# Kernel optimization log

Measured on AMD Instinct MI355X. Metric: run time of the kernel, lower is better.

Reference implementation:

```python
import jax, jax.numpy as jnp
import numpy as np

NUM_ITEMS = 5
DIM = 1024
BATCH = 2048
NUM_PAIR = NUM_ITEMS * (NUM_ITEMS - 1)  # 20
NUM_RESULTS = 120  # 5!

# Off-diagonal ordered pairs in row-major flatten order (i*N + j, i != j).
_mask = ~np.eye(NUM_ITEMS, dtype=bool)
_IDX_I, _IDX_J = np.nonzero(_mask)  # each length NUM_PAIR
IDX_I = jnp.asarray(_IDX_I)
IDX_J = jnp.asarray(_IDX_J)


def setup_inputs() -> dict:
    key = jax.random.key(0)
    k1, k2, k3, k4, k5 = jax.random.split(key, 5)
    s_pw = 1.0 / np.sqrt(2 * DIM)
    s_cls = 1.0 / np.sqrt(NUM_PAIR * DIM)
    return {
        "embeds": jax.random.normal(k1, (BATCH, NUM_ITEMS, DIM), dtype=jnp.float32),
        "pw_w": jax.random.uniform(k2, (DIM, 2 * DIM), dtype=jnp.float32, minval=-s_pw, maxval=s_pw),
        "pw_b": jax.random.uniform(k3, (DIM,), dtype=jnp.float32, minval=-s_pw, maxval=s_pw),
        "cls_w": jax.random.uniform(k4, (NUM_RESULTS, NUM_PAIR * DIM), dtype=jnp.float32, minval=-s_cls, maxval=s_cls),
        "cls_b": jax.random.uniform(k5, (NUM_RESULTS,), dtype=jnp.float32, minval=-s_cls, maxval=s_cls),
    }


def reference(embeds, pw_w, pw_b, cls_w, cls_b):
    # Gather the two halves of each ordered off-diagonal pair directly
    # (equivalent to expand/cat/mask-select in the torch code).
    e_i = embeds[:, IDX_I, :]  # [B, P, D] : rep_1 (row item)
    e_j = embeds[:, IDX_J, :]  # [B, P, D] : rep_2 (col item)
    # pairwise_layer on concat(e_i, e_j): split weight to avoid the cat.
    w1 = pw_w[:, :DIM]
    w2 = pw_w[:, DIM:]
    pair = jnp.einsum('bpd,kd->bpk', e_i, w1) + jnp.einsum('bpd,kd->bpk', e_j, w2) + pw_b  # [B, P, D]
    flat = pair.reshape(pair.shape[0], -1)  # [B, P*D]
    return flat @ cls_w.T + cls_b  # [B, NUM_RESULTS]
```

## Files before the change

### kernel.cpp

```cpp
#include <hip/hip_runtime.h>


#define NR 120
#define KXX 5120
#define PM_SLICE (2048*128)
#define PF_SLICE (128*5120)

typedef __attribute__((ext_vector_type(8))) short bf8;
typedef __attribute__((ext_vector_type(4))) float f4;

__device__ __forceinline__ unsigned int f2bf(float f) {
    unsigned int x = __builtin_bit_cast(unsigned int, f);
    return (x + 0x7fffu + ((x >> 16) & 1u)) >> 16;
}
__device__ __forceinline__ float bf2f(unsigned short u) {
    unsigned int x = ((unsigned int)u) << 16;
    return __builtin_bit_cast(float, x);
}

__global__ __launch_bounds__(256) void k_prep(const float* __restrict__ cls_w,
                                              unsigned short* __restrict__ C2R) {
    const int col = blockIdx.x, half = blockIdx.y, t = threadIdx.x;
    const int n = col >> 7, r = col & 127;
    unsigned short* dst = C2R + (size_t)col * 2048 + half * 1024 + t * 4;
    if (r >= NR) { *(unsigned long long*)dst = 0ull; return; }
    const float* base = cls_w + (size_t)r * 20480 + t * 4;
    float sx = 0, sy = 0, sz = 0, sw = 0;
    if (half == 0) {
        #pragma unroll
        for (int q = 0; q < 4; q++) {
            float4 v = *(const float4*)(base + (4 * n + q) * 1024);
            sx += v.x; sy += v.y; sz += v.z; sw += v.w;
        }
    } else {
        #pragma unroll
        for (int i = 0; i < 5; i++) {
            if (i == n) continue;
            int q = (n > i) ? (n - 1) : n;
            float4 v = *(const float4*)(base + (4 * i + q) * 1024);
            sx += v.x; sy += v.y; sz += v.z; sw += v.w;
        }
    }
    unsigned long long pk = (unsigned long long)f2bf(sx)
                          | ((unsigned long long)f2bf(sy) << 16)
                          | ((unsigned long long)f2bf(sz) << 32)
                          | ((unsigned long long)f2bf(sw) << 48);
    *(unsigned long long*)dst = pk;
}

__global__ __launch_bounds__(256) void k_wprep(const float* __restrict__ pw_w,
                                               unsigned short* __restrict__ Afold) {
    __shared__ float T[64][65];
    const int d0 = blockIdx.x * 64, kt0 = blockIdx.y * 64;
    const int h = blockIdx.y >> 4, kr0 = (blockIdx.y & 15) * 64;
    const int t = threadIdx.x;
    #pragma unroll
    for (int lp = 0; lp < 4; lp++) {
        int lk = lp * 16 + (t >> 4);
        float4 v = *(const float4*)(pw_w + (size_t)(kr0 + lk) * 2048 + h * 1024 + d0 + (t & 15) * 4);
        T[lk][(t & 15) * 4 + 0] = v.x; T[lk][(t & 15) * 4 + 1] = v.y;
        T[lk][(t & 15) * 4 + 2] = v.z; T[lk][(t & 15) * 4 + 3] = v.w;
    }
    __syncthreads();
    #pragma unroll
    for (int wp = 0; wp < 2; wp++) {
        int ld = wp * 32 + (t >> 3);
        int lk2 = (t & 7) * 8;
        uint4 o;
        o.x = f2bf(T[lk2 + 0][ld]) | (f2bf(T[lk2 + 1][ld]) << 16);
        o.y = f2bf(T[lk2 + 2][ld]) | (f2bf(T[lk2 + 3][ld]) << 16);
        o.z = f2bf(T[lk2 + 4][ld]) | (f2bf(T[lk2 + 5][ld]) << 16);
        o.w = f2bf(T[lk2 + 6][ld]) | (f2bf(T[lk2 + 7][ld]) << 16);
        *(uint4*)(Afold + (size_t)(d0 + ld) * 2048 + kt0 + lk2) = o;
    }
}

__global__ __launch_bounds__(256) void k_const(const unsigned short* __restrict__ C2R,
                                               const float* __restrict__ pw_b,
                                               const float* __restrict__ cls_b,
                                               float* __restrict__ constv) {
    const int r = blockIdx.x, t = threadIdx.x;
    float acc = 0.f;
    for (int k = t; k < 1024; k += 256) {
        float s = 0.f;
        #pragma unroll
        for (int n = 0; n < 5; n++) s += bf2f(C2R[(size_t)(n * 128 + r) * 2048 + k]);
        acc += s * pw_b[k];
    }
    __shared__ float red[256];
    red[t] = acc; __syncthreads();
    for (int s2 = 128; s2 > 0; s2 >>= 1) {
        if (t < s2) red[t] += red[t + s2];
        __syncthreads();
    }
    if (t == 0) constv[r] = cls_b[r] + red[0];
}

__global__ __launch_bounds__(256) void k_fold(const unsigned short* __restrict__ Afold,
                                              const unsigned short* __restrict__ C2R,
                                              float* __restrict__ Pf, int kchunk) {
    __shared__ __align__(16) unsigned char smem[65536];
    unsigned short* Al = (unsigned short*)smem;
    unsigned short* Bl = Al + 128 * 64;
    const int d0 = blockIdx.x * 128, n = blockIdx.y;
    const int kc0 = blockIdx.z * kchunk;
    const int t = threadIdx.x, lane = t & 63, wv = t >> 6;
    const int wm = wv >> 1, wn = wv & 1;
    const int rr = t >> 3, f = t & 7;

    f4 acc[4][4];
    #pragma unroll
    for (int i = 0; i < 4; i++)
        #pragma unroll
        for (int j = 0; j < 4; j++) acc[i][j] = (f4){0.f, 0.f, 0.f, 0.f};

    const unsigned short* Ag = Afold + (size_t)d0 * 2048 + kc0;
    const unsigned short* Bg = C2R + (size_t)(n * 128) * 2048 + kc0;
    uint4 ra[4], rb[4];
    #pragma unroll
    for (int p = 0; p < 4; p++) {
        ra[p] = *(const uint4*)(Ag + (size_t)(p * 32 + rr) * 2048 + f * 8);
        rb[p] = *(const uint4*)(Bg + (size_t)(p * 32 + rr) * 2048 + f * 8);
    }
    const int nst = kchunk >> 6;
    for (int kt = 0; kt < nst; kt++) {
        if (kt) __syncthreads();
        #pragma unroll
        for (int p = 0; p < 4; p++) {
            int row = p * 32 + rr;
            int slot = f ^ (row & 7);
            *(uint4*)(Al + row * 64 + slot * 8) = ra[p];
            *(uint4*)(Bl + row * 64 + slot * 8) = rb[p];
        }
        __syncthreads();
        if (kt + 1 < nst) {
            int kb = (kt + 1) * 64;
            #pragma unroll
            for (int p = 0; p < 4; p++) {
                ra[p] = *(const uint4*)(Ag + (size_t)(p * 32 + rr) * 2048 + kb + f * 8);
                rb[p] = *(const uint4*)(Bg + (size_t)(p * 32 + rr) * 2048 + kb + f * 8);
            }
        }
        #pragma unroll
        for (int s = 0; s < 2; s++) {
            bf8 af[4], bq[4];
            #pragma unroll
            for (int ff = 0; ff < 4; ff++) {
                int rowa = wm * 64 + ff * 16 + (lane & 15);
                int sla = (s * 4 + (lane >> 4)) ^ (rowa & 7);
                af[ff] = *reinterpret_cast<const bf8*>(Al + rowa * 64 + sla * 8);
                int rowb = wn * 64 + ff * 16 + (lane & 15);
                int slb = (s * 4 + (lane >> 4)) ^ (rowb & 7);
                bq[ff] = *reinterpret_cast<const bf8*>(Bl + rowb * 64 + slb * 8);
            }
            #pragma unroll
            for (int i = 0; i < 4; i++)
                #pragma unroll
                for (int j = 0; j < 4; j++)
                    acc[i][j] = __builtin_amdgcn_mfma_f32_16x16x32_bf16(af[i], bq[j], acc[i][j], 0, 0, 0);
        }
    }
    __syncthreads();
    float* T = (float*)smem;
    #pragma unroll
    for (int i = 0; i < 4; i++) {
        int slog = wm * 16 + i * 4 + (lane >> 4);
        #pragma unroll
        for (int j = 0; j < 4; j++) {
            int c = wn * 64 + j * 16 + (lane & 15);
            int sphy = slog ^ ((c & 7) << 2);
            *(f4*)(T + (size_t)c * 128 + sphy * 4) = acc[i][j];
        }
    }
    __syncthreads();
    float* dst = Pf + (size_t)blockIdx.z * PF_SLICE + n * 1024 + d0;
    #pragma unroll
    for (int pass = 0; pass < 4; pass++) {
        int c = pass * 32 + (t >> 3);
        #pragma unroll
        for (int u = 0; u < 4; u++) {
            int slog = (t & 7) + u * 8;
            int sphy = slog ^ ((c & 7) << 2);
            float4 v = *(const float4*)(T + (size_t)c * 128 + sphy * 4);
            *(float4*)(dst + (size_t)c * KXX + slog * 4) = v;
        }
    }
}

__global__ __launch_bounds__(256) void k_foldred(const float* __restrict__ Pf,
                                                 unsigned short* __restrict__ WTt,
                                                 int ksf) {
    int i4 = blockIdx.x * 256 + threadIdx.x;
    const float4* p = (const float4*)Pf;
    float4 s = p[i4];
    for (int ks = 1; ks < ksf; ks++) {
        float4 v = p[(size_t)ks * (PF_SLICE / 4) + i4];
        s.x += v.x; s.y += v.y; s.z += v.z; s.w += v.w;
    }
    unsigned long long pk = (unsigned long long)f2bf(s.x)
                          | ((unsigned long long)f2bf(s.y) << 16)
                          | ((unsigned long long)f2bf(s.z) << 32)
                          | ((unsigned long long)f2bf(s.w) << 48);
    *(unsigned long long*)(WTt + (size_t)i4 * 4) = pk;
}

__global__ __launch_bounds__(256) void k_main(const float* __restrict__ E,
                                              const unsigned short* __restrict__ WTt,
                                              float* __restrict__ Pm, int kchunk) {
    __shared__ __align__(16) unsigned short lds[2 * 128 * 64];
    unsigned short* Al = lds;
    unsigned short* Bl = lds + 128 * 64;
    const int m0 = blockIdx.x * 128;
    const int kc0 = blockIdx.y * kchunk;
    const int t = threadIdx.x, lane = t & 63, wv = t >> 6;
    const int wm = wv >> 1, wn = wv & 1;
    const int rr = t >> 3, f = t & 7;

    f4 acc[4][4];
    #pragma unroll
    for (int i = 0; i < 4; i++)
        #pragma unroll
        for (int j = 0; j < 4; j++) acc[i][j] = (f4){0.f, 0.f, 0.f, 0.f};

    const float* Ag = E + (size_t)m0 * KXX + kc0;
    const unsigned short* Bg = WTt + kc0;
    float4 raA[2][4][2];
    uint4 raB[2][4];
    const int nst = kchunk >> 6;
    #pragma unroll
    for (int st = 0; st < 2; st++) {
        int kb = st * 64;
        #pragma unroll
        for (int p = 0; p < 4; p++) {
            const float* a = Ag + (size_t)(p * 32 + rr) * KXX + kb + f * 8;
            raA[st][p][0] = *(const float4*)a;
            raA[st][p][1] = *(const float4*)(a + 4);
            raB[st][p] = *(const uint4*)(Bg + (size_t)(p * 32 + rr) * KXX + kb + f * 8);
        }
    }
    for (int kt = 0; kt < nst; kt++) {
        const int par = kt & 1;
        if (kt) __syncthreads();
        #pragma unroll
        for (int p = 0; p < 4; p++) {
            int row = p * 32 + rr;
            int slot = f ^ (row & 7);
            float4 v0 = raA[par][p][0], v1 = raA[par][p][1];
            uint4 o;
            o.x = f2bf(v0.x) | (f2bf(v0.y) << 16);
            o.y = f2bf(v0.z) | (f2bf(v0.w) << 16);
            o.z = f2bf(v1.x) | (f2bf(v1.y) << 16);
            o.w = f2bf(v1.z) | (f2bf(v1.w) << 16);
            *(uint4*)(Al + row * 64 + slot * 8) = o;
            *(uint4*)(Bl + row * 64 + slot * 8) = raB[par][p];
        }
        __syncthreads();
        if (kt + 2 < nst) {
            int kb = (kt + 2) * 64;
            #pragma unroll
            for (int p = 0; p < 4; p++) {
                const float* a = Ag + (size_t)(p * 32 + rr) * KXX + kb + f * 8;
                raA[par][p][0] = *(const float4*)a;
                raA[par][p][1] = *(const float4*)(a + 4);
                raB[par][p] = *(const uint4*)(Bg + (size_t)(p * 32 + rr) * KXX + kb + f * 8);
            }
        }
        #pragma unroll
        for (int s = 0; s < 2; s++) {
            bf8 af[4], bq[4];
            #pragma unroll
            for (int ff = 0; ff < 4; ff++) {
                int rowa = wm * 64 + ff * 16 + (lane & 15);
                int sla = (s * 4 + (lane >> 4)) ^ (rowa & 7);
                af[ff] = *reinterpret_cast<const bf8*>(Al + rowa * 64 + sla * 8);
                int rowb = wn * 64 + ff * 16 + (lane & 15);
                int slb = (s * 4 + (lane >> 4)) ^ (rowb & 7);
                bq[ff] = *reinterpret_cast<const bf8*>(Bl + rowb * 64 + slb * 8);
            }
            #pragma unroll
            for (int i = 0; i < 4; i++)
                #pragma unroll
                for (int j = 0; j < 4; j++)
                    acc[i][j] = __builtin_amdgcn_mfma_f32_16x16x32_bf16(af[i], bq[j], acc[i][j], 0, 0, 0);
        }
    }
    float* dst = Pm + (size_t)blockIdx.y * PM_SLICE;
    #pragma unroll
    for (int i = 0; i < 4; i++) {
        int row = m0 + wm * 64 + i * 16 + (lane >> 4) * 4;
        #pragma unroll
        for (int j = 0; j < 4; j++) {
            int col = wn * 64 + j * 16 + (lane & 15);
            #pragma unroll
            for (int q = 0; q < 4; q++)
                dst[(size_t)(row + q) * 128 + col] = acc[i][j][q];
        }
    }
}

__global__ __launch_bounds__(256) void k_mainred(const float* __restrict__ Pm,
                                                 const float* __restrict__ constv,
                                                 float* __restrict__ out, int nksm) {
    int tid = blockIdx.x * 256 + threadIdx.x;
    int b = tid / NR, r = tid - b * NR;
    float s = constv[r];
    for (int ks = 0; ks < nksm; ks++)
        s += Pm[(size_t)ks * PM_SLICE + (size_t)b * 128 + r];
    out[tid] = s;
}

extern "C" void kernel_launch(void* const* d_in, const int* in_sizes, int n_in,
                              void* d_out, int out_size, void* d_ws, size_t ws_size,
                              hipStream_t stream) {
    const float* embeds = (const float*)d_in[0];
    const float* pw_w   = (const float*)d_in[1];
    const float* pw_b   = (const float*)d_in[2];
    const float* cls_w  = (const float*)d_in[3];
    const float* cls_b  = (const float*)d_in[4];
    float* out = (float*)d_out;

    unsigned short* C2R   = (unsigned short*)d_ws;
    unsigned short* Afold = C2R + (size_t)640 * 2048;
    unsigned short* WTt   = Afold + (size_t)1024 * 2048;
    float* constv = (float*)(WTt + (size_t)128 * 5120);
    float* scratch = constv + 128;

    size_t base = ((size_t)640 * 2048 + (size_t)1024 * 2048 + (size_t)128 * 5120) * 2 + 512;
    size_t avail = (ws_size > base) ? (ws_size - base) / 4 : 0;
    const int candm[6] = {20, 16, 8, 4, 2, 1};
    int nksm = 1;
    for (int ci = 0; ci < 6; ci++)
        if ((size_t)candm[ci] * PM_SLICE <= avail) { nksm = candm[ci]; break; }
    const int candf[4] = {8, 4, 2, 1};
    int ksf = 1;
    for (int ci = 0; ci < 4; ci++)
        if ((size_t)candf[ci] * PF_SLICE <= avail) { ksf = candf[ci]; break; }

    k_prep<<<dim3(640, 2), dim3(256), 0, stream>>>(cls_w, C2R);
    k_wprep<<<dim3(16, 32), dim3(256), 0, stream>>>(pw_w, Afold);
    k_const<<<dim3(NR), dim3(256), 0, stream>>>(C2R, pw_b, cls_b, constv);
    k_fold<<<dim3(8, 5, ksf), dim3(256), 0, stream>>>(Afold, C2R, scratch, 2048 / ksf);
    k_foldred<<<dim3(640), dim3(256), 0, stream>>>(scratch, WTt, ksf);
    k_main<<<dim3(16, nksm), dim3(256), 0, stream>>>(embeds, WTt, scratch, KXX / nksm);
    k_mainred<<<dim3(960), dim3(256), 0, stream>>>(scratch, constv, out, nksm);
}
```

Before: 201.5 us.

## Halve M tile in fold and main GEMMs, stage main output via LDS

Both the fold GEMM and the main GEMM now use 64-row M tiles instead of 128, which doubles the grid (16x5xksf and 32xnksm) so more CUs are busy on this small problem. The main GEMM stages its accumulators through padded LDS so the partials go out as coalesced float4 stores, and the split-K count for the main GEMM is capped at 16. k_const now reads fp32 cls_w directly, so it no longer depends on the prep kernel and runs first. Smaller tiles lower the MFMA-to-load ratio and raise the amount of global traffic per FLOP.

```diff
diff --git a/kernel.cpp b/kernel.cpp
--- a/kernel.cpp
+++ b/kernel.cpp
@@ -75,16 +75,17 @@
     }
 }
 
-__global__ __launch_bounds__(256) void k_const(const unsigned short* __restrict__ C2R,
+__global__ __launch_bounds__(256) void k_const(const float* __restrict__ cls_w,
                                                const float* __restrict__ pw_b,
                                                const float* __restrict__ cls_b,
                                                float* __restrict__ constv) {
     const int r = blockIdx.x, t = threadIdx.x;
+    const float* base = cls_w + (size_t)r * 20480;
     float acc = 0.f;
     for (int k = t; k < 1024; k += 256) {
         float s = 0.f;
         #pragma unroll
-        for (int n = 0; n < 5; n++) s += bf2f(C2R[(size_t)(n * 128 + r) * 2048 + k]);
+        for (int p = 0; p < 20; p++) s += base[p * 1024 + k];
         acc += s * pw_b[k];
     }
     __shared__ float red[256];
@@ -99,62 +100,73 @@
 __global__ __launch_bounds__(256) void k_fold(const unsigned short* __restrict__ Afold,
                                               const unsigned short* __restrict__ C2R,
                                               float* __restrict__ Pf, int kchunk) {
-    __shared__ __align__(16) unsigned char smem[65536];
+    __shared__ __align__(16) unsigned char smem[34048];
     unsigned short* Al = (unsigned short*)smem;
-    unsigned short* Bl = Al + 128 * 64;
-    const int d0 = blockIdx.x * 128, n = blockIdx.y;
+    unsigned short* Bl = (unsigned short*)(smem + 8192);
+    const int d0 = blockIdx.x * 64, n = blockIdx.y;
     const int kc0 = blockIdx.z * kchunk;
     const int t = threadIdx.x, lane = t & 63, wv = t >> 6;
     const int wm = wv >> 1, wn = wv & 1;
     const int rr = t >> 3, f = t & 7;
 
-    f4 acc[4][4];
-    #pragma unroll
-    for (int i = 0; i < 4; i++)
+    f4 acc[2][4];
+    #pragma unroll
+    for (int i = 0; i < 2; i++)
         #pragma unroll
         for (int j = 0; j < 4; j++) acc[i][j] = (f4){0.f, 0.f, 0.f, 0.f};
 
     const unsigned short* Ag = Afold + (size_t)d0 * 2048 + kc0;
     const unsigned short* Bg = C2R + (size_t)(n * 128) * 2048 + kc0;
-    uint4 ra[4], rb[4];
-    #pragma unroll
-    for (int p = 0; p < 4; p++) {
+    uint4 ra[2], rb[4];
+    #pragma unroll
+    for (int p = 0; p < 2; p++)
         ra[p] = *(const uint4*)(Ag + (size_t)(p * 32 + rr) * 2048 + f * 8);
+    #pragma unroll
+    for (int p = 0; p < 4; p++)
         rb[p] = *(const uint4*)(Bg + (size_t)(p * 32 + rr) * 2048 + f * 8);
-    }
+
     const int nst = kchunk >> 6;
     for (int kt = 0; kt < nst; kt++) {
         if (kt) __syncthreads();
         #pragma unroll
+        for (int p = 0; p < 2; p++) {
+            int row = p * 32 + rr;
+            int slot = f ^ (row & 7);
+            *(uint4*)(Al + row * 64 + slot * 8) = ra[p];
+        }
+        #pragma unroll
         for (int p = 0; p < 4; p++) {
             int row = p * 32 + rr;
             int slot = f ^ (row & 7);
-            *(uint4*)(Al + row * 64 + slot * 8) = ra[p];
             *(uint4*)(Bl + row * 64 + slot * 8) = rb[p];
         }
         __syncthreads();
         if (kt + 1 < nst) {
             int kb = (kt + 1) * 64;
             #pragma unroll
-            for (int p = 0; p < 4; p++) {
+            for (int p = 0; p < 2; p++)
                 ra[p] = *(const uint4*)(Ag + (size_t)(p * 32 + rr) * 2048 + kb + f * 8);
+            #pragma unroll
+            for (int p = 0; p < 4; p++)
                 rb[p] = *(const uint4*)(Bg + (size_t)(p * 32 + rr) * 2048 + kb + f * 8);
-            }
         }
         #pragma unroll
         for (int s = 0; s < 2; s++) {
-            bf8 af[4], bq[4];
-            #pragma unroll
-            for (int ff = 0; ff < 4; ff++) {
-                int rowa = wm * 64 + ff * 16 + (lane & 15);
+            bf8 af[2], bq[4];
+            #pragma unroll
+            for (int ff = 0; ff < 2; ff++) {
+                int rowa = wm * 32 + ff * 16 + (lane & 15);
                 int sla = (s * 4 + (lane >> 4)) ^ (rowa & 7);
                 af[ff] = *reinterpret_cast<const bf8*>(Al + rowa * 64 + sla * 8);
+            }
+            #pragma unroll
+            for (int ff = 0; ff < 4; ff++) {
                 int rowb = wn * 64 + ff * 16 + (lane & 15);
                 int slb = (s * 4 + (lane >> 4)) ^ (rowb & 7);
                 bq[ff] = *reinterpret_cast<const bf8*>(Bl + rowb * 64 + slb * 8);
             }
             #pragma unroll
-            for (int i = 0; i < 4; i++)
+            for (int i = 0; i < 2; i++)
                 #pragma unroll
                 for (int j = 0; j < 4; j++)
                     acc[i][j] = __builtin_amdgcn_mfma_f32_16x16x32_bf16(af[i], bq[j], acc[i][j], 0, 0, 0);
@@ -163,13 +175,13 @@
     __syncthreads();
     float* T = (float*)smem;
     #pragma unroll
-    for (int i = 0; i < 4; i++) {
-        int slog = wm * 16 + i * 4 + (lane >> 4);
+    for (int i = 0; i < 2; i++) {
+        int s16 = wm * 8 + i * 4 + (lane >> 4);
         #pragma unroll
         for (int j = 0; j < 4; j++) {
             int c = wn * 64 + j * 16 + (lane & 15);
-            int sphy = slog ^ ((c & 7) << 2);
-            *(f4*)(T + (size_t)c * 128 + sphy * 4) = acc[i][j];
+            int sphy = s16 ^ (c & 15);
+            *(f4*)(T + (size_t)c * 64 + sphy * 4) = acc[i][j];
         }
     }
     __syncthreads();
@@ -178,10 +190,10 @@
     for (int pass = 0; pass < 4; pass++) {
         int c = pass * 32 + (t >> 3);
         #pragma unroll
-        for (int u = 0; u < 4; u++) {
+        for (int u = 0; u < 2; u++) {
             int slog = (t & 7) + u * 8;
-            int sphy = slog ^ ((c & 7) << 2);
-            float4 v = *(const float4*)(T + (size_t)c * 128 + sphy * 4);
+            int sphy = slog ^ (c & 15);
+            float4 v = *(const float4*)(T + (size_t)c * 64 + sphy * 4);
             *(float4*)(dst + (size_t)c * KXX + slog * 4) = v;
         }
     }
@@ -207,93 +219,111 @@
 __global__ __launch_bounds__(256) void k_main(const float* __restrict__ E,
                                               const unsigned short* __restrict__ WTt,
                                               float* __restrict__ Pm, int kchunk) {
-    __shared__ __align__(16) unsigned short lds[2 * 128 * 64];
-    unsigned short* Al = lds;
-    unsigned short* Bl = lds + 128 * 64;
-    const int m0 = blockIdx.x * 128;
+    __shared__ __align__(16) unsigned char smem[34048];
+    unsigned short* Al = (unsigned short*)smem;
+    unsigned short* Bl = (unsigned short*)(smem + 8192);
+    const int m0 = blockIdx.x * 64;
     const int kc0 = blockIdx.y * kchunk;
     const int t = threadIdx.x, lane = t & 63, wv = t >> 6;
     const int wm = wv >> 1, wn = wv & 1;
-    const int rr = t >> 3, f = t & 7;
-
-    f4 acc[4][4];
-    #pragma unroll
-    for (int i = 0; i < 4; i++)
+    const int rrb = t >> 3, f = t & 7;
+    const int rra = t >> 2, fa = t & 3;
+
+    f4 acc[2][4];
+    #pragma unroll
+    for (int i = 0; i < 2; i++)
         #pragma unroll
         for (int j = 0; j < 4; j++) acc[i][j] = (f4){0.f, 0.f, 0.f, 0.f};
 
     const float* Ag = E + (size_t)m0 * KXX + kc0;
     const unsigned short* Bg = WTt + kc0;
-    float4 raA[2][4][2];
+    float4 raA[2][4];
     uint4 raB[2][4];
     const int nst = kchunk >> 6;
     #pragma unroll
     for (int st = 0; st < 2; st++) {
         int kb = st * 64;
         #pragma unroll
-        for (int p = 0; p < 4; p++) {
-            const float* a = Ag + (size_t)(p * 32 + rr) * KXX + kb + f * 8;
-            raA[st][p][0] = *(const float4*)a;
-            raA[st][p][1] = *(const float4*)(a + 4);
-            raB[st][p] = *(const uint4*)(Bg + (size_t)(p * 32 + rr) * KXX + kb + f * 8);
-        }
+        for (int u = 0; u < 4; u++)
+            raA[st][u] = *(const float4*)(Ag + (size_t)rra * KXX + kb + fa * 16 + u * 4);
+        #pragma unroll
+        for (int p = 0; p < 4; p++)
+            raB[st][p] = *(const uint4*)(Bg + (size_t)(p * 32 + rrb) * KXX + kb + f * 8);
     }
     for (int kt = 0; kt < nst; kt++) {
         const int par = kt & 1;
         if (kt) __syncthreads();
         #pragma unroll
-        for (int p = 0; p < 4; p++) {
-            int row = p * 32 + rr;
-            int slot = f ^ (row & 7);
-            float4 v0 = raA[par][p][0], v1 = raA[par][p][1];
+        for (int u = 0; u < 2; u++) {
+            float4 v0 = raA[par][2 * u], v1 = raA[par][2 * u + 1];
             uint4 o;
             o.x = f2bf(v0.x) | (f2bf(v0.y) << 16);
             o.y = f2bf(v0.z) | (f2bf(v0.w) << 16);
             o.z = f2bf(v1.x) | (f2bf(v1.y) << 16);
             o.w = f2bf(v1.z) | (f2bf(v1.w) << 16);
-            *(uint4*)(Al + row * 64 + slot * 8) = o;
+            int slot = (fa * 2 + u) ^ (rra & 7);
+            *(uint4*)(Al + rra * 64 + slot * 8) = o;
+        }
+        #pragma unroll
+        for (int p = 0; p < 4; p++) {
+            int row = p * 32 + rrb;
+            int slot = f ^ (row & 7);
             *(uint4*)(Bl + row * 64 + slot * 8) = raB[par][p];
         }
         __syncthreads();
         if (kt + 2 < nst) {
             int kb = (kt + 2) * 64;
             #pragma unroll
-            for (int p = 0; p < 4; p++) {
-                const float* a = Ag + (size_t)(p * 32 + rr) * KXX + kb + f * 8;
-                raA[par][p][0] = *(const float4*)a;
-                raA[par][p][1] = *(const float4*)(a + 4);
-                raB[par][p] = *(const uint4*)(Bg + (size_t)(p * 32 + rr) * KXX + kb + f * 8);
-            }
+            for (int u = 0; u < 4; u++)
+                raA[par][u] = *(const float4*)(Ag + (size_t)rra * KXX + kb + fa * 16 + u * 4);
+            #pragma unroll
+            for (int p = 0; p < 4; p++)
+                raB[par][p] = *(const uint4*)(Bg + (size_t)(p * 32 + rrb) * KXX + kb + f * 8);
         }
         #pragma unroll
         for (int s = 0; s < 2; s++) {
-            bf8 af[4], bq[4];
-            #pragma unroll
-            for (int ff = 0; ff < 4; ff++) {
-                int rowa = wm * 64 + ff * 16 + (lane & 15);
+            bf8 af[2], bq[4];
+            #pragma unroll
+            for (int ff = 0; ff < 2; ff++) {
+                int rowa = wm * 32 + ff * 16 + (lane & 15);
                 int sla = (s * 4 + (lane >> 4)) ^ (rowa & 7);
                 af[ff] = *reinterpret_cast<const bf8*>(Al + rowa * 64 + sla * 8);
+            }
+            #pragma unroll
+            for (int ff = 0; ff < 4; ff++) {
                 int rowb = wn * 64 + ff * 16 + (lane & 15);
                 int slb = (s * 4 + (lane >> 4)) ^ (rowb & 7);
                 bq[ff] = *reinterpret_cast<const bf8*>(Bl + rowb * 64 + slb * 8);
             }
             #pragma unroll
-            for (int i = 0; i < 4; i++)
+            for (int i = 0; i < 2; i++)
                 #pragma unroll
                 for (int j = 0; j < 4; j++)
                     acc[i][j] = __builtin_amdgcn_mfma_f32_16x16x32_bf16(af[i], bq[j], acc[i][j], 0, 0, 0);
         }
     }
-    float* dst = Pm + (size_t)blockIdx.y * PM_SLICE;
-    #pragma unroll
-    for (int i = 0; i < 4; i++) {
-        int row = m0 + wm * 64 + i * 16 + (lane >> 4) * 4;
+    __syncthreads();
+    float* T2 = (float*)smem;
+    #pragma unroll
+    for (int i = 0; i < 2; i++) {
+        int rowb = wm * 32 + i * 16 + (lane >> 4) * 4;
         #pragma unroll
         for (int j = 0; j < 4; j++) {
-            int col = wn * 64 + j * 16 + (lane & 15);
+            int colr = wn * 64 + j * 16 + (lane & 15);
             #pragma unroll
             for (int q = 0; q < 4; q++)
-                dst[(size_t)(row + q) * 128 + col] = acc[i][j][q];
+                T2[(size_t)(rowb + q) * 132 + colr] = acc[i][j][q];
+        }
+    }
+    __syncthreads();
+    float* dst = Pm + (size_t)blockIdx.y * PM_SLICE + (size_t)m0 * 128;
+    {
+        int row = t >> 2;
+        int cb = (t & 3) * 32;
+        #pragma unroll
+        for (int u = 0; u < 8; u++) {
+            int c = cb + u * 4;
+            *(float4*)(dst + (size_t)row * 128 + c) = *(const float4*)(T2 + (size_t)row * 132 + c);
         }
     }
 }
@@ -327,20 +357,20 @@
 
     size_t base = ((size_t)640 * 2048 + (size_t)1024 * 2048 + (size_t)128 * 5120) * 2 + 512;
     size_t avail = (ws_size > base) ? (ws_size - base) / 4 : 0;
-    const int candm[6] = {20, 16, 8, 4, 2, 1};
+    const int candm[5] = {16, 8, 4, 2, 1};
     int nksm = 1;
-    for (int ci = 0; ci < 6; ci++)
+    for (int ci = 0; ci < 5; ci++)
         if ((size_t)candm[ci] * PM_SLICE <= avail) { nksm = candm[ci]; break; }
     const int candf[4] = {8, 4, 2, 1};
     int ksf = 1;
     for (int ci = 0; ci < 4; ci++)
         if ((size_t)candf[ci] * PF_SLICE <= avail) { ksf = candf[ci]; break; }
 
+    k_const<<<dim3(NR), dim3(256), 0, stream>>>(cls_w, pw_b, cls_b, constv);
     k_prep<<<dim3(640, 2), dim3(256), 0, stream>>>(cls_w, C2R);
     k_wprep<<<dim3(16, 32), dim3(256), 0, stream>>>(pw_w, Afold);
-    k_const<<<dim3(NR), dim3(256), 0, stream>>>(C2R, pw_b, cls_b, constv);
-    k_fold<<<dim3(8, 5, ksf), dim3(256), 0, stream>>>(Afold, C2R, scratch, 2048 / ksf);
+    k_fold<<<dim3(16, 5, ksf), dim3(256), 0, stream>>>(Afold, C2R, scratch, 2048 / ksf);
     k_foldred<<<dim3(640), dim3(256), 0, stream>>>(scratch, WTt, ksf);
-    k_main<<<dim3(16, nksm), dim3(256), 0, stream>>>(embeds, WTt, scratch, KXX / nksm);
+    k_main<<<dim3(32, nksm), dim3(256), 0, stream>>>(embeds, WTt, scratch, KXX / nksm);
     k_mainred<<<dim3(960), dim3(256), 0, stream>>>(scratch, constv, out, nksm);
 }
```

Measured after the change: 179.7 us. -10.8%, faster.
